# Optimization experiments

Measured on AMD Instinct MI355X. Metric: run time of the kernel, lower is better.

The kernel has to match this reference:

```python
import jax, jax.numpy as jnp
import numpy as np

NEG_SLOPE = 0.2  # PyG GATv2Conv default negative_slope


def segment_softmax(scores, dst, num_nodes):
    # scores: [E, H], softmax over edges sharing the same destination node
    m = jax.ops.segment_max(scores, dst, num_segments=num_nodes)  # [N, H]
    e = jnp.exp(scores - m[dst])
    s = jax.ops.segment_sum(e, dst, num_segments=num_nodes)  # [N, H]
    return e / (s[dst] + 1e-16)


def gatv2_conv(x, src, dst, Wl, bl, Wr, br, att, bias, heads, out_ch, concat):
    # PyG GATv2: x_l = lin_l(x) used for source/messages, x_r = lin_r(x) for target
    n = x.shape[0]
    xl = (x @ Wl + bl).reshape(n, heads, out_ch)
    xr = (x @ Wr + br).reshape(n, heads, out_ch)
    e = jax.nn.leaky_relu(xl[src] + xr[dst], NEG_SLOPE)        # [E, H, C]
    score = jnp.einsum('ehc,hc->eh', e, att)                    # [E, H]
    alpha = segment_softmax(score, dst, n)                      # [E, H]
    msg = xl[src] * alpha[..., None]                            # [E, H, C]
    out = jax.ops.segment_sum(msg, dst, num_segments=n)         # [N, H, C]
    out = out.reshape(n, heads * out_ch) if concat else out.mean(axis=1)
    return out + bias


def setup_inputs() -> dict:
    key = jax.random.key(0)
    ks = jax.random.split(key, 20)
    N, F_IN, H, C = 50000, 256, 4, 64
    E = 600000
    x = jax.random.normal(ks[0], (N, F_IN), dtype=jnp.float32)
    edge_index = jax.random.randint(ks[1], (2, E), 0, N, dtype=jnp.int64)

    def glorot(k, shape):
        fan_in = shape[0]
        return jax.random.normal(k, shape, dtype=jnp.float32) / jnp.sqrt(jnp.float32(fan_in))

    params = dict(
        # layer 1: in=256, heads=4, out=64, concat -> 256
        W1l=glorot(ks[2], (F_IN, H * C)), b1l=jnp.zeros((H * C,), jnp.float32),
        W1r=glorot(ks[3], (F_IN, H * C)), b1r=jnp.zeros((H * C,), jnp.float32),
        att1=glorot(ks[4], (H, C)), bias1=jnp.zeros((H * C,), jnp.float32),
        # layer 2: in=256, heads=1, out=64, no concat
        W2l=glorot(ks[5], (H * C, C)), b2l=jnp.zeros((C,), jnp.float32),
        W2r=glorot(ks[6], (H * C, C)), b2r=jnp.zeros((C,), jnp.float32),
        att2=glorot(ks[7], (1, C)), bias2=jnp.zeros((C,), jnp.float32),
        # predict head: 64 -> 32 -> 1
        Wp1=glorot(ks[8], (C, 32)), bp1=jnp.zeros((32,), jnp.float32),
        Wp2=glorot(ks[9], (32, 1)), bp2=jnp.zeros((1,), jnp.float32),
    )
    return {'x': x, 'edge_index': edge_index, **params}


def reference(x, edge_index, W1l, b1l, W1r, b1r, att1, bias1,
              W2l, b2l, W2r, b2r, att2, bias2, Wp1, bp1, Wp2, bp2):
    n = x.shape[0]
    # PyG GATv2Conv default add_self_loops=True
    loop = jnp.arange(n, dtype=edge_index.dtype)
    src = jnp.concatenate([edge_index[0], loop])
    dst = jnp.concatenate([edge_index[1], loop])

    h = gatv2_conv(x, src, dst, W1l, b1l, W1r, b1r, att1, bias1,
                   heads=4, out_ch=64, concat=True)
    h = jax.nn.leaky_relu(h, 0.01)  # F.leaky_relu default slope
    h = gatv2_conv(h, src, dst, W2l, b2l, W2r, b2r, att2, bias2,
                   heads=1, out_ch=64, concat=False)
    z = jax.nn.leaky_relu(h @ Wp1 + bp1, 0.01)
    logits = z @ Wp2 + bp2
    return logits, h
```

## Files before the change

### kernel.cpp

```cpp
#include <hip/hip_runtime.h>

typedef __attribute__((ext_vector_type(8))) __bf16 bf16x8;
typedef __attribute__((ext_vector_type(4))) float f32x4;

#define EXP2 __builtin_amdgcn_exp2f
#define LOG2E 1.44269504f
#define MFMA __builtin_amdgcn_mfma_f32_16x16x32_bf16

__device__ __forceinline__ float lrelu(float v, float s) { return v > 0.f ? v : v * s; }

__device__ __forceinline__ unsigned short f2bf(float f) {
    unsigned int u = __float_as_uint(f);
    u += 0x7FFFu + ((u >> 16) & 1u);
    return (unsigned short)(u >> 16);
}
__device__ __forceinline__ float bf2f(unsigned short u) {
    return __uint_as_float((unsigned int)u << 16);
}

__device__ __forceinline__ int ld_idx(const int* p, int e, int is64) {
    return is64 ? (int)(((const long long*)p)[e]) : p[e];
}

__global__ void detect_i64(const unsigned int* idx, int* flag) {
    if (blockIdx.x == 0 && threadIdx.x == 0) {
        int all0 = 1;
        for (int i = 1; i < 256; i += 2) {
            if (idx[i] != 0u) { all0 = 0; break; }
        }
        *flag = all0;
    }
}

__global__ void convert_all(const float* __restrict__ x,
                            const float* __restrict__ W1l, const float* __restrict__ W1r,
                            const float* __restrict__ W2l, const float* __restrict__ W2r,
                            unsigned short* __restrict__ xb,
                            unsigned short* __restrict__ w1t, unsigned short* __restrict__ w2t,
                            int n, int nrb)
{
    int t = blockIdx.x * blockDim.x + threadIdx.x;
    int A = nrb * 512;
    if (t < A) {
        int lane = t & 63;
        int kf = (t >> 6) & 7;
        int rowblk = t >> 9;
        int r16 = lane & 15, kg = lane >> 4;
        int row = rowblk * 16 + r16;
        int k0 = kf * 32 + kg * 8;
        ushort4 o0 = {0, 0, 0, 0}, o1 = {0, 0, 0, 0};
        if (row < n) {
            float4 v0 = *(const float4*)(x + (size_t)row * 256 + k0);
            float4 v1 = *(const float4*)(x + (size_t)row * 256 + k0 + 4);
            o0.x = f2bf(v0.x); o0.y = f2bf(v0.y); o0.z = f2bf(v0.z); o0.w = f2bf(v0.w);
            o1.x = f2bf(v1.x); o1.y = f2bf(v1.y); o1.z = f2bf(v1.z); o1.w = f2bf(v1.w);
        }
        *(ushort4*)(xb + (size_t)t * 8) = o0;
        *(ushort4*)(xb + (size_t)t * 8 + 4) = o1;
        return;
    }
    int tw = t - A;
    const float *Wl, *Wr;
    unsigned short* dst;
    int NL, base;
    if (tw < 16384)      { Wl = W1l; Wr = W1r; dst = w1t; NL = 256; base = tw; }
    else if (tw < 20480) { Wl = W2l; Wr = W2r; dst = w2t; NL = 64;  base = tw - 16384; }
    else return;
    int lane = base & 63, kf = (base >> 6) & 7, colblk = base >> 9;
    int r16 = lane & 15, kg = lane >> 4;
    int col = colblk * 16 + r16;
    int k0 = kf * 32 + kg * 8;
    const float* W = (col < NL) ? Wl : Wr;
    int c = (col < NL) ? col : col - NL;
    unsigned short v[8];
#pragma unroll
    for (int e = 0; e < 8; e++) v[e] = f2bf(W[(size_t)(k0 + e) * NL + c]);
    ushort4 o0 = {v[0], v[1], v[2], v[3]}, o1 = {v[4], v[5], v[6], v[7]};
    *(ushort4*)(dst + (size_t)base * 8) = o0;
    *(ushort4*)(dst + (size_t)base * 8 + 4) = o1;
}

template <int N, int K, int RB, int WCB>
__global__ __launch_bounds__(256) void gemm_frag(
    const unsigned short* __restrict__ A, const unsigned short* __restrict__ Bt,
    const float* __restrict__ biasL, const float* __restrict__ biasR, int NL,
    unsigned short* __restrict__ C, int M, int nrb)
{
    constexpr int KF = K / 32;
    int wid = threadIdx.x >> 6, lane = threadIdx.x & 63;
    int wm = wid >> 1, wn = wid & 1;
    int rbase = (blockIdx.x * 2 + wm) * RB;
    int cb0 = blockIdx.y * (2 * WCB) + wn * WCB;
    const unsigned short* Ap[RB];
#pragma unroll
    for (int r = 0; r < RB; r++) {
        int rb = min(rbase + r, nrb - 1);
        Ap[r] = A + ((size_t)rb * KF * 64 + lane) * 8;
    }
    const unsigned short* B0 = Bt + ((size_t)cb0 * KF * 64 + lane) * 8;
    f32x4 acc[RB][WCB] = {};
#pragma unroll
    for (int kf = 0; kf < KF; kf++) {
        bf16x8 a[RB];
#pragma unroll
        for (int r = 0; r < RB; r++) a[r] = *(const bf16x8*)(Ap[r] + kf * 512);
#pragma unroll
        for (int j = 0; j < WCB; j++) {
            bf16x8 b = *(const bf16x8*)(B0 + (size_t)j * KF * 512 + kf * 512);
#pragma unroll
            for (int r = 0; r < RB; r++) acc[r][j] = MFMA(a[r], b, acc[r][j], 0, 0, 0);
        }
    }
    int ccol = lane & 15, crow = (lane >> 4) * 4;
#pragma unroll
    for (int r = 0; r < RB; r++) {
#pragma unroll
        for (int j = 0; j < WCB; j++) {
            int col = (cb0 + j) * 16 + ccol;
            float bv = (col < NL) ? biasL[col] : biasR[col - NL];
#pragma unroll
            for (int q = 0; q < 4; q++) {
                int row = (rbase + r) * 16 + crow + q;
                if (row < M) C[(size_t)row * N + col] = f2bf(acc[r][j][q] + bv);
            }
        }
    }
}

__global__ void hist_dst_pos(const int* __restrict__ eidx, const int* __restrict__ flagp,
                             int E, int n, int* __restrict__ cnt, int* __restrict__ pos)
{
    int t = blockIdx.x * blockDim.x + threadIdx.x;
    if (t >= E + n) return;
    int is64 = *flagp;
    int d = (t < E) ? ld_idx(eidx, E + t, is64) : (t - E);
    pos[t] = atomicAdd(&cnt[d], 1);
}

__global__ __launch_bounds__(1024) void scan1(const int* __restrict__ cnt,
                                              int* __restrict__ rowptr, int* __restrict__ psum, int n)
{
    __shared__ int wsum[16];
    int tid = threadIdx.x, lane = tid & 63, w = tid >> 6;
    int gid = blockIdx.x * 1024 + tid;
    int v = (gid < n) ? cnt[gid] : 0;
    int sc = v;
#pragma unroll
    for (int o = 1; o < 64; o <<= 1) { int t2 = __shfl_up(sc, o); if (lane >= o) sc += t2; }
    if (lane == 63) wsum[w] = sc;
    __syncthreads();
    if (tid < 16) {
        int t2 = wsum[tid];
#pragma unroll
        for (int o = 1; o < 16; o <<= 1) { int u = __shfl_up(t2, o); if (tid >= o) t2 += u; }
        wsum[tid] = t2;
    }
    __syncthreads();
    int wofs = w ? wsum[w - 1] : 0;
    if (gid < n) rowptr[gid] = wofs + sc - v;
    if (tid == 1023) psum[blockIdx.x] = wsum[15];
}

__global__ void scan2(const int* __restrict__ psum, int* __restrict__ pofs,
                      int* __restrict__ rowptr_n, int nb)
{
    int lane = threadIdx.x;
    int v = (lane < nb) ? psum[lane] : 0;
    int sc = v;
#pragma unroll
    for (int o = 1; o < 64; o <<= 1) { int t = __shfl_up(sc, o); if (lane >= o) sc += t; }
    if (lane < nb) pofs[lane] = sc - v;
    if (lane == 63) *rowptr_n = sc;
}

__global__ __launch_bounds__(1024) void scan3(int* __restrict__ rowptr,
                                              const int* __restrict__ pofs, int n)
{
    int gid = blockIdx.x * 1024 + threadIdx.x;
    if (gid < n) rowptr[gid] += pofs[blockIdx.x];
}

__global__ void scatter_pos(const int* __restrict__ eidx, const int* __restrict__ flagp,
                            int E, int n, const int* __restrict__ rowptr,
                            const int* __restrict__ pos, int* __restrict__ sord)
{
    int t = blockIdx.x * blockDim.x + threadIdx.x;
    if (t >= E + n) return;
    int is64 = *flagp;
    int s, d;
    if (t < E) { s = ld_idx(eidx, t, is64); d = ld_idx(eidx, E + t, is64); }
    else { s = t - E; d = s; }
    sord[rowptr[d] + pos[t]] = s;
}

#define SCOREX(p, xv) { float t_; p = 0.f;                              \
    t_ = xv.x + xrv.x; p = fmaf(t_, a6.x, p); p = fmaf(fabsf(t_), a4.x, p); \
    t_ = xv.y + xrv.y; p = fmaf(t_, a6.y, p); p = fmaf(fabsf(t_), a4.y, p); \
    t_ = xv.z + xrv.z; p = fmaf(t_, a6.z, p); p = fmaf(fabsf(t_), a4.z, p); \
    t_ = xv.w + xrv.w; p = fmaf(t_, a6.w, p); p = fmaf(fabsf(t_), a4.w, p); }

#define RED16(p) { p += __shfl_xor(p, 1); p += __shfl_xor(p, 2);    \
                   p += __shfl_xor(p, 4); p += __shfl_xor(p, 8); }

#define EACC(v, xv) { float ev = EXP2(v); ssum += ev;                \
    o.x = fmaf(ev, xv.x, o.x); o.y = fmaf(ev, xv.y, o.y);            \
    o.z = fmaf(ev, xv.z, o.z); o.w = fmaf(ev, xv.w, o.w); }

#define CVT4(f, u) float4 f = { bf2f(u.x), bf2f(u.y), bf2f(u.z), bf2f(u.w) };

__global__ __launch_bounds__(256) void node_attn_h4(
    const unsigned short* __restrict__ xlr,
    const float* __restrict__ att, const float* __restrict__ bias,
    const int* __restrict__ rowptr, const int* __restrict__ sord, int n,
    unsigned short* __restrict__ outb)
{
    int d = (blockIdx.x * blockDim.x + threadIdx.x) >> 6;
    int lane = threadIdx.x & 63;
    if (d >= n) return;
    int off = (lane >> 4) * 64 + (lane & 15) * 4;
    ushort4 xru = *(const ushort4*)(xlr + (size_t)d * 512 + 256 + off);
    CVT4(xrv, xru);
    float4 atv = *(const float4*)(att + off);
    float4 a6, a4;
    a6.x = atv.x * (0.6f * LOG2E); a6.y = atv.y * (0.6f * LOG2E);
    a6.z = atv.z * (0.6f * LOG2E); a6.w = atv.w * (0.6f * LOG2E);
    a4.x = atv.x * (0.4f * LOG2E); a4.y = atv.y * (0.4f * LOG2E);
    a4.z = atv.z * (0.4f * LOG2E); a4.w = atv.w * (0.4f * LOG2E);
    int beg = rowptr[d], end = rowptr[d + 1];
    float ssum = 0.f;
    float4 o = {0.f, 0.f, 0.f, 0.f};
    for (int i = beg; i < end; i += 4) {
        int i1 = i + 1, i2 = i + 2, i3 = i + 3;
        int v1 = i1 < end, v2 = i2 < end, v3 = i3 < end;
        int s0 = sord[i];
        int s1 = sord[v1 ? i1 : i];
        int s2 = sord[v2 ? i2 : i];
        int s3 = sord[v3 ? i3 : i];
        ushort4 u0 = *(const ushort4*)(xlr + (size_t)s0 * 512 + off);
        ushort4 u1 = *(const ushort4*)(xlr + (size_t)s1 * 512 + off);
        ushort4 u2 = *(const ushort4*)(xlr + (size_t)s2 * 512 + off);
        ushort4 u3 = *(const ushort4*)(xlr + (size_t)s3 * 512 + off);
        CVT4(x0, u0); CVT4(x1, u1); CVT4(x2, u2); CVT4(x3, u3);
        float p0, p1, p2, p3;
        SCOREX(p0, x0); SCOREX(p1, x1); SCOREX(p2, x2); SCOREX(p3, x3);
        RED16(p0); RED16(p1); RED16(p2); RED16(p3);
        p1 = v1 ? p1 : -1e30f;
        p2 = v2 ? p2 : -1e30f;
        p3 = v3 ? p3 : -1e30f;
        EACC(p0, x0); EACC(p1, x1); EACC(p2, x2); EACC(p3, x3);
    }
    float inv = 1.f / (ssum + 1e-16f);
    float4 bv = *(const float4*)(bias + off);
    float r0 = o.x * inv + bv.x, r1 = o.y * inv + bv.y;
    float r2 = o.z * inv + bv.z, r3 = o.w * inv + bv.w;
    r0 = fmaxf(r0, 0.01f * r0); r1 = fmaxf(r1, 0.01f * r1);
    r2 = fmaxf(r2, 0.01f * r2); r3 = fmaxf(r3, 0.01f * r3);
    ushort4 ov;
    ov.x = f2bf(r0); ov.y = f2bf(r1); ov.z = f2bf(r2); ov.w = f2bf(r3);
    int rowblk = d >> 4, r16d = d & 15;
    int kf = off >> 5, kg2 = (off >> 3) & 3, e0 = off & 7;
    size_t flat = (((size_t)rowblk * 8 + kf) * 64 + kg2 * 16 + r16d) * 8 + e0;
    *(ushort4*)(outb + flat) = ov;
}

__global__ __launch_bounds__(256) void node_attn_h1(
    const unsigned short* __restrict__ xlr,
    const float* __restrict__ att, const float* __restrict__ bias,
    const int* __restrict__ rowptr, const int* __restrict__ sord, int n,
    float* __restrict__ outf)
{
    int d = (blockIdx.x * blockDim.x + threadIdx.x) >> 6;
    int lane = threadIdx.x & 63;
    if (d >= n) return;
    int sg = lane >> 4, c0 = (lane & 15) * 4;
    ushort4 xru = *(const ushort4*)(xlr + (size_t)d * 128 + 64 + c0);
    CVT4(xrv, xru);
    float4 atv = *(const float4*)(att + c0);
    float4 a6, a4;
    a6.x = atv.x * (0.6f * LOG2E); a6.y = atv.y * (0.6f * LOG2E);
    a6.z = atv.z * (0.6f * LOG2E); a6.w = atv.w * (0.6f * LOG2E);
    a4.x = atv.x * (0.4f * LOG2E); a4.y = atv.y * (0.4f * LOG2E);
    a4.z = atv.z * (0.4f * LOG2E); a4.w = atv.w * (0.4f * LOG2E);
    int beg = rowptr[d], end = rowptr[d + 1];
    float ssum = 0.f;
    float4 o = {0.f, 0.f, 0.f, 0.f};
    for (int i0 = beg; i0 < end; i0 += 8) {
        int ia = i0 + sg, ib = i0 + 4 + sg;
        int va = ia < end, vb = ib < end;
        int sa = sord[va ? ia : beg];
        int sb = sord[vb ? ib : beg];
        ushort4 ua = *(const ushort4*)(xlr + (size_t)sa * 128 + c0);
        ushort4 ub = *(const ushort4*)(xlr + (size_t)sb * 128 + c0);
        CVT4(xa, ua); CVT4(xb, ub);
        float pa, pb;
        SCOREX(pa, xa); SCOREX(pb, xb);
        RED16(pa); RED16(pb);
        pa = va ? pa : -1e30f;
        pb = vb ? pb : -1e30f;
        EACC(pa, xa); EACC(pb, xb);
    }
#pragma unroll
    for (int offs = 16; offs <= 32; offs <<= 1) {
        ssum += __shfl_xor(ssum, offs);
        o.x += __shfl_xor(o.x, offs); o.y += __shfl_xor(o.y, offs);
        o.z += __shfl_xor(o.z, offs); o.w += __shfl_xor(o.w, offs);
    }
    if (sg == 0) {
        float inv = 1.f / (ssum + 1e-16f);
        float4 bv = *(const float4*)(bias + c0);
        float4 res;
        res.x = o.x * inv + bv.x; res.y = o.y * inv + bv.y;
        res.z = o.z * inv + bv.z; res.w = o.w * inv + bv.w;
        *(float4*)(outf + (size_t)d * 64 + c0) = res;
    }
}

__global__ void predict_head(const float* __restrict__ h2,
                             const float* __restrict__ Wp1, const float* __restrict__ bp1,
                             const float* __restrict__ Wp2, const float* __restrict__ bp2,
                             float* __restrict__ logits, int n)
{
    int i = blockIdx.x * blockDim.x + threadIdx.x;
    if (i >= n) return;
    float h[64];
#pragma unroll
    for (int c = 0; c < 64; c++) h[c] = h2[(long long)i * 64 + c];
    float logit = bp2[0];
#pragma unroll
    for (int j = 0; j < 32; j++) {
        float z = bp1[j];
#pragma unroll
        for (int c = 0; c < 64; c++) z += h[c] * Wp1[c * 32 + j];
        z = lrelu(z, 0.01f);
        logit += z * Wp2[j];
    }
    logits[i] = logit;
}

extern "C" void kernel_launch(void* const* d_in, const int* in_sizes, int n_in,
                              void* d_out, int out_size, void* d_ws, size_t ws_size,
                              hipStream_t stream)
{
    const float* x    = (const float*)d_in[0];
    const int*   eidx = (const int*)d_in[1];
    const float* W1l  = (const float*)d_in[2];
    const float* b1l  = (const float*)d_in[3];
    const float* W1r  = (const float*)d_in[4];
    const float* b1r  = (const float*)d_in[5];
    const float* att1 = (const float*)d_in[6];
    const float* bias1= (const float*)d_in[7];
    const float* W2l  = (const float*)d_in[8];
    const float* b2l  = (const float*)d_in[9];
    const float* W2r  = (const float*)d_in[10];
    const float* b2r  = (const float*)d_in[11];
    const float* att2 = (const float*)d_in[12];
    const float* bias2= (const float*)d_in[13];
    const float* Wp1  = (const float*)d_in[14];
    const float* bp1  = (const float*)d_in[15];
    const float* Wp2  = (const float*)d_in[16];
    const float* bp2  = (const float*)d_in[17];

    const int n = in_sizes[0] / 256;
    const int E = in_sizes[1] / 2;
    const int Etot = E + n;
    const int nb = (n + 1023) / 1024;
    const int nrb = (n + 15) / 16;

    float* out = (float*)d_out;
    unsigned short* ws16 = (unsigned short*)d_ws;

    unsigned short* xb    = ws16;
    unsigned short* xlr1  = xb + (size_t)nrb * 4096;
    unsigned short* w1t   = xlr1 + (size_t)n * 512;
    unsigned short* w2t   = w1t + 131072;
    int*            rowptr= (int*)(w2t + 32768);
    int*            cnt   = rowptr + (n + 1);
    int*            sord  = cnt + n;
    int*            pos   = sord + Etot;
    int*            psum  = pos + Etot;
    int*            pofs  = psum + 64;
    int*            flagp = pofs + 64;
    unsigned short* h1b   = xb;
    unsigned short* xlr2  = xlr1;
    float*          h2    = out + n;

    detect_i64<<<1, 64, 0, stream>>>((const unsigned int*)eidx, flagp);

    hipMemsetAsync(cnt, 0, (size_t)n * sizeof(int), stream);
    hist_dst_pos<<<(Etot + 255) / 256, 256, 0, stream>>>(eidx, flagp, E, n, cnt, pos);
    scan1<<<nb, 1024, 0, stream>>>(cnt, rowptr, psum, n);
    scan2<<<1, 64, 0, stream>>>(psum, pofs, rowptr + n, nb);
    scan3<<<nb, 1024, 0, stream>>>(rowptr, pofs, n);
    scatter_pos<<<(Etot + 255) / 256, 256, 0, stream>>>(eidx, flagp, E, n, rowptr, pos, sord);

    convert_all<<<(nrb * 512 + 20480 + 255) / 256, 256, 0, stream>>>(
        x, W1l, W1r, W2l, W2r, xb, w1t, w2t, n, nrb);

    {
        dim3 grid((nrb + 7) / 8, 2);
        gemm_frag<512, 256, 4, 8><<<grid, 256, 0, stream>>>(xb, w1t, b1l, b1r, 256, xlr1, n, nrb);
    }

    node_attn_h4<<<(n + 3) / 4, 256, 0, stream>>>(xlr1, att1, bias1, rowptr, sord, n, h1b);

    {
        dim3 grid((nrb + 3) / 4, 1);
        gemm_frag<128, 256, 2, 4><<<grid, 256, 0, stream>>>(h1b, w2t, b2l, b2r, 64, xlr2, n, nrb);
    }

    node_attn_h1<<<(n + 3) / 4, 256, 0, stream>>>(xlr2, att2, bias2, rowptr, sord, n, h2);

    predict_head<<<(n + 255) / 256, 256, 0, stream>>>(h2, Wp1, bp1, Wp2, bp2, out, n);
}
```

Before: 249.2 us.

## Stage GEMM fragments through double-buffered LDS via global_load_lds

Replaces the register-direct fragment GEMM with a kernel that copies A and B fragments into double-buffered shared memory using global_load_lds, then every wave reads its 4x4 MFMA tiles from LDS. A block now covers 8 row-blocks by 8 column-blocks and shares those loads across its four waves, which is meant to cut redundant global loads and overlap the next k-step's load with the current step's MFMAs. The cost is a block barrier every k-step and a retuned grid (more blocks along columns for layer 1, larger row tiles for layer 2).

```diff
diff --git a/kernel.cpp b/kernel.cpp
--- a/kernel.cpp
+++ b/kernel.cpp
@@ -6,6 +6,10 @@
 #define EXP2 __builtin_amdgcn_exp2f
 #define LOG2E 1.44269504f
 #define MFMA __builtin_amdgcn_mfma_f32_16x16x32_bf16
+
+#define GLL(srcp, dstp) __builtin_amdgcn_global_load_lds( \
+    (const __attribute__((address_space(1))) void*)(srcp), \
+    (__attribute__((address_space(3))) void*)(dstp), 16, 0, 0)
 
 __device__ __forceinline__ float lrelu(float v, float s) { return v > 0.f ? v : v * s; }
 
@@ -80,47 +84,66 @@
     *(ushort4*)(dst + (size_t)base * 8 + 4) = o1;
 }
 
-template <int N, int K, int RB, int WCB>
-__global__ __launch_bounds__(256) void gemm_frag(
+template <int KF>
+__global__ __launch_bounds__(256) void gemm_lds(
     const unsigned short* __restrict__ A, const unsigned short* __restrict__ Bt,
     const float* __restrict__ biasL, const float* __restrict__ biasR, int NL,
-    unsigned short* __restrict__ C, int M, int nrb)
-{
-    constexpr int KF = K / 32;
+    unsigned short* __restrict__ C, int M, int nrb, int N)
+{
+    __shared__ unsigned short lds[2][16 * 512];
     int wid = threadIdx.x >> 6, lane = threadIdx.x & 63;
     int wm = wid >> 1, wn = wid & 1;
-    int rbase = (blockIdx.x * 2 + wm) * RB;
-    int cb0 = blockIdx.y * (2 * WCB) + wn * WCB;
-    const unsigned short* Ap[RB];
-#pragma unroll
-    for (int r = 0; r < RB; r++) {
-        int rb = min(rbase + r, nrb - 1);
-        Ap[r] = A + ((size_t)rb * KF * 64 + lane) * 8;
-    }
-    const unsigned short* B0 = Bt + ((size_t)cb0 * KF * 64 + lane) * 8;
-    f32x4 acc[RB][WCB] = {};
-#pragma unroll
+    int rb0 = blockIdx.x * 8;
+    int cb0 = blockIdx.y * 8;
+
+    auto stage = [&](int buf, int kf) {
+#pragma unroll
+        for (int i = 0; i < 4; i++) {
+            int c = wid * 4 + i;
+            const unsigned short* src;
+            if (c < 8) {
+                int rb = rb0 + c;
+                rb = rb < nrb ? rb : nrb - 1;
+                src = A + ((size_t)rb * KF + kf) * 512;
+            } else {
+                src = Bt + ((size_t)(cb0 + c - 8) * KF + kf) * 512;
+            }
+            GLL(src + lane * 8, &lds[buf][c * 512]);
+        }
+    };
+
+    f32x4 acc[4][4] = {};
+    stage(0, 0);
+    __syncthreads();
+    int cur = 0;
     for (int kf = 0; kf < KF; kf++) {
-        bf16x8 a[RB];
-#pragma unroll
-        for (int r = 0; r < RB; r++) a[r] = *(const bf16x8*)(Ap[r] + kf * 512);
-#pragma unroll
-        for (int j = 0; j < WCB; j++) {
-            bf16x8 b = *(const bf16x8*)(B0 + (size_t)j * KF * 512 + kf * 512);
-#pragma unroll
-            for (int r = 0; r < RB; r++) acc[r][j] = MFMA(a[r], b, acc[r][j], 0, 0, 0);
-        }
-    }
+        if (kf + 1 < KF) stage(cur ^ 1, kf + 1);
+        bf16x8 a[4], b[4];
+#pragma unroll
+        for (int r = 0; r < 4; r++)
+            a[r] = *(const bf16x8*)&lds[cur][(wm * 4 + r) * 512 + lane * 8];
+#pragma unroll
+        for (int j = 0; j < 4; j++)
+            b[j] = *(const bf16x8*)&lds[cur][(8 + wn * 4 + j) * 512 + lane * 8];
+#pragma unroll
+        for (int j = 0; j < 4; j++)
+#pragma unroll
+            for (int r = 0; r < 4; r++)
+                acc[r][j] = MFMA(a[r], b[j], acc[r][j], 0, 0, 0);
+        __syncthreads();
+        cur ^= 1;
+    }
+
     int ccol = lane & 15, crow = (lane >> 4) * 4;
 #pragma unroll
-    for (int r = 0; r < RB; r++) {
-#pragma unroll
-        for (int j = 0; j < WCB; j++) {
-            int col = (cb0 + j) * 16 + ccol;
+    for (int r = 0; r < 4; r++) {
+#pragma unroll
+        for (int j = 0; j < 4; j++) {
+            int col = (cb0 + wn * 4 + j) * 16 + ccol;
             float bv = (col < NL) ? biasL[col] : biasR[col - NL];
 #pragma unroll
             for (int q = 0; q < 4; q++) {
-                int row = (rbase + r) * 16 + crow + q;
+                int row = (rb0 + wm * 4 + r) * 16 + crow + q;
                 if (row < M) C[(size_t)row * N + col] = f2bf(acc[r][j][q] + bv);
             }
         }
@@ -397,15 +420,15 @@
         x, W1l, W1r, W2l, W2r, xb, w1t, w2t, n, nrb);
 
     {
-        dim3 grid((nrb + 7) / 8, 2);
-        gemm_frag<512, 256, 4, 8><<<grid, 256, 0, stream>>>(xb, w1t, b1l, b1r, 256, xlr1, n, nrb);
+        dim3 grid((nrb + 7) / 8, 4);
+        gemm_lds<8><<<grid, 256, 0, stream>>>(xb, w1t, b1l, b1r, 256, xlr1, n, nrb, 512);
     }
 
     node_attn_h4<<<(n + 3) / 4, 256, 0, stream>>>(xlr1, att1, bias1, rowptr, sord, n, h1b);
 
     {
-        dim3 grid((nrb + 3) / 4, 1);
-        gemm_frag<128, 256, 2, 4><<<grid, 256, 0, stream>>>(h1b, w2t, b2l, b2r, 64, xlr2, n, nrb);
+        dim3 grid((nrb + 7) / 8, 1);
+        gemm_lds<8><<<grid, 256, 0, stream>>>(h1b, w2t, b2l, b2r, 64, xlr2, n, nrb, 128);
     }
 
     node_attn_h1<<<(n + 3) / 4, 256, 0, stream>>>(xlr2, att2, bias2, rowptr, sord, n, h2);
```

Result: faster. 226.7 us (median of 2 runs) (-9.0%).
